# Optimization experiments

Measured on AMD Instinct MI355X. Metric: run time of the kernel, lower is better.

## Reference

```python
import jax, jax.numpy as jnp
import numpy as np

N = 100000      # nodes
K = 16          # sampled neighbors per node (aggregate_num)
D = 256         # features_dim
DO = 256        # out_feat_dim
ALPHA = 0.2     # LeakyReLU negative slope (args.alpha)
EPS = 1e-12     # F.normalize eps


def setup_inputs() -> dict:
    key = jax.random.key(0)
    k1, k2, k3 = jax.random.split(key, 3)
    h = jax.random.normal(k1, (N, D), dtype=jnp.float32)
    neighbors = jax.random.randint(k2, (N, K), 0, N, dtype=jnp.int64)
    # Xavier-uniform-ish init for W_gcn
    limit = float(np.sqrt(6.0 / (D + DO)))
    W_gcn = jax.random.uniform(k3, (D, DO), dtype=jnp.float32, minval=-limit, maxval=limit)
    return {"h": h, "neighbors": neighbors, "W_gcn": W_gcn}


def reference(h, neighbors, W_gcn):
    # GCN-style aggregate: mean of self feature and K sampled neighbor features.
    # (dropout on neighbor feats is identity in eval mode)
    neigh_sum = jnp.sum(h[neighbors], axis=1)          # [N, D] gather + reduce
    agg = (h + neigh_sum) / jnp.float32(K + 1)         # [N, D]
    z = agg @ W_gcn                                    # [N, DO]
    z = jnp.where(z >= 0, z, ALPHA * z)                # LeakyReLU
    norm = jnp.sqrt(jnp.sum(z * z, axis=1, keepdims=True))
    return z / jnp.maximum(norm, EPS)                  # L2 normalize per row
```

## Files before the change

kernel.cpp:

```cpp
#include <hip/hip_runtime.h>
#include <stdint.h>

#define N_NODES 100000
#define KNBR 16
#define ALPHA 0.2f

typedef __attribute__((ext_vector_type(8))) short bf16x8;
typedef __attribute__((ext_vector_type(4))) float f32x4;
typedef __attribute__((ext_vector_type(4))) unsigned int u32x4;
typedef unsigned short u16;
typedef unsigned int u32;
typedef unsigned char u8;

static __device__ __forceinline__ u16 f2bf(float f) {
  u32 u = __builtin_bit_cast(u32, f);
  u += 0x7fffu + ((u >> 16) & 1u);
  return (u16)(u >> 16);
}

__global__ __launch_bounds__(256) void prep_w_kernel(const float* __restrict__ W,
                                                     u16* __restrict__ Wb) {
  const int t = blockIdx.x * 256 + threadIdx.x;
  const int l = t & 63;
  const int ct = (t >> 6) & 15;
  const int ks = t >> 10;
  const int colbase = ct * 16 + (l & 15);
  const int k0 = ks * 32 + (l >> 4) * 8;
  u32 wq[4];
#pragma unroll
  for (int q = 0; q < 4; ++q) {
    const u16 b0 = f2bf(W[(k0 + 2 * q) * 256 + colbase]);
    const u16 b1 = f2bf(W[(k0 + 2 * q + 1) * 256 + colbase]);
    wq[q] = (u32)b0 | ((u32)b1 << 16);
  }
  u32x4 o = {wq[0], wq[1], wq[2], wq[3]};
  *(u32x4*)(Wb + (size_t)t * 8) = o;
}

__global__ __launch_bounds__(256, 4) void gemm_kernel(const float* __restrict__ h,
                                                      const u16* __restrict__ Wb,
                                                      u8* __restrict__ Yq,
                                                      float* __restrict__ scale) {
  __shared__ __align__(16) u16 aS[32 * 256];
  __shared__ float redS[4][32];
  __shared__ float invSS[32];
  const int tid = threadIdx.x;
  const int blk = blockIdx.x;
  const size_t base = (size_t)blk * (32 * 256);

#pragma unroll
  for (int i = 0; i < 8; ++i) {
    const int flat = i * 1024 + tid * 4;
    const int row = flat >> 8, d0 = flat & 255;
    const f32x4 v = __builtin_nontemporal_load((const f32x4*)(h + base + flat));
    uint2 o;
    asm("v_cvt_pk_bf16_f32 %0, %1, %2" : "=v"(o.x) : "v"(v[0]), "v"(v[1]));
    asm("v_cvt_pk_bf16_f32 %0, %1, %2" : "=v"(o.y) : "v"(v[2]), "v"(v[3]));
    *(uint2*)((char*)aS + row * 512 + ((d0 * 2) ^ ((row & 7) << 4))) = o;
  }
  __syncthreads();

  const int l = tid & 63, wv = tid >> 6;
  const int l15 = l & 15, lg = l >> 4;
  f32x4 acc[2][4] = {};
  const u32x4* wbL = ((const u32x4*)Wb) + (size_t)(wv * 4) * 64 + l;
  const char* aggB = (const char*)aS;
  const int rb0 = l15 * 512;
  const int xm = (l15 & 7) << 4;
#pragma unroll 2
  for (int ks = 0; ks < 8; ++ks) {
    const int offk = ((ks * 64) + lg * 16) ^ xm;
    const bf16x8 a0 = *(const bf16x8*)(aggB + rb0 + offk);
    const bf16x8 a1 = *(const bf16x8*)(aggB + rb0 + 8192 + offk);
#pragma unroll
    for (int c = 0; c < 4; ++c) {
      const u32x4 bw = wbL[ks * 1024 + c * 64];
      const bf16x8 b = __builtin_bit_cast(bf16x8, bw);
      acc[0][c] = __builtin_amdgcn_mfma_f32_16x16x32_bf16(a0, b, acc[0][c], 0, 0, 0);
      acc[1][c] = __builtin_amdgcn_mfma_f32_16x16x32_bf16(a1, b, acc[1][c], 0, 0, 0);
    }
  }

#pragma unroll
  for (int rt = 0; rt < 2; ++rt)
#pragma unroll
    for (int j = 0; j < 4; ++j) {
      float m = 0.f;
#pragma unroll
      for (int c = 0; c < 4; ++c) m = fmaxf(m, fabsf(acc[rt][c][j]));
      m = fmaxf(m, __shfl_xor(m, 1)); m = fmaxf(m, __shfl_xor(m, 2));
      m = fmaxf(m, __shfl_xor(m, 4)); m = fmaxf(m, __shfl_xor(m, 8));
      redS[wv][rt * 16 + lg * 4 + j] = m;
    }
  __syncthreads();
  if (tid < 32) {
    float m = fmaxf(fmaxf(redS[0][tid], redS[1][tid]),
                    fmaxf(redS[2][tid], redS[3][tid]));
    m = fmaxf(m, 1e-20f);
    scale[blk * 32 + tid] = m * (1.0f / 127.0f);
    invSS[tid] = 127.0f / m;
  }
  __syncthreads();

  u8* qS = (u8*)aS;
#pragma unroll
  for (int rt = 0; rt < 2; ++rt)
#pragma unroll
    for (int j = 0; j < 4; ++j) {
      const int r = rt * 16 + lg * 4 + j;
      const float inv = invSS[r];
      const int sw = ((r >> 2) & 7) << 5;
#pragma unroll
      for (int c = 0; c < 4; ++c) {
        float t = fmaf(acc[rt][c][j], inv, 128.5f);
        t = fminf(255.f, fmaxf(1.f, t));
        qS[r * 256 + ((wv * 64 + c * 16 + l15) ^ sw)] = (u8)(u32)t;
      }
    }
  __syncthreads();

  const u32x4* q4 = (const u32x4*)aS;
  u32x4* yg = (u32x4*)(Yq + (size_t)blk * 8192);
#pragma unroll
  for (int q = 0; q < 2; ++q) {
    const int f = q * 4096 + tid * 16;
    const int row = f >> 8, col = f & 255;
    const int colx = col ^ (((row >> 2) & 7) << 5);
    __builtin_nontemporal_store(q4[(row * 256 + colx) >> 4], (u32x4*)&yg[f >> 4]);
  }
}

__global__ __launch_bounds__(256) void gather_kernel(const u8* __restrict__ Yq,
                                                     const float* __restrict__ scale,
                                                     const int* __restrict__ nbr,
                                                     float* __restrict__ out) {
  const int tid = threadIdx.x;
  const int lane = tid & 63, wv = tid >> 6;
  const int node = __builtin_amdgcn_readfirstlane(blockIdx.x * 4 + wv);

  const int il = nbr[node * KNBR + (lane & 15)];
  const float vscale = scale[il];
  const float sself = scale[node];
  const u32* yb = (const u32*)Yq;

  u32 v[17];
  v[0] = yb[(size_t)node * 64 + lane];
#pragma unroll
  for (int j = 0; j < 16; ++j) {
    const int r = __builtin_amdgcn_readlane(il, j);
    v[j + 1] = yb[(size_t)r * 64 + lane];
  }

  float a0, a1, a2, a3, S = sself;
  {
    float f0, f1, f2, f3;
    asm("v_cvt_f32_ubyte0 %0, %1" : "=v"(f0) : "v"(v[0]));
    asm("v_cvt_f32_ubyte1 %0, %1" : "=v"(f1) : "v"(v[0]));
    asm("v_cvt_f32_ubyte2 %0, %1" : "=v"(f2) : "v"(v[0]));
    asm("v_cvt_f32_ubyte3 %0, %1" : "=v"(f3) : "v"(v[0]));
    a0 = sself * f0; a1 = sself * f1; a2 = sself * f2; a3 = sself * f3;
  }
#pragma unroll
  for (int j = 0; j < 16; ++j) {
    const float s = __builtin_bit_cast(
        float, __builtin_amdgcn_readlane(__builtin_bit_cast(int, vscale), j));
    float f0, f1, f2, f3;
    asm("v_cvt_f32_ubyte0 %0, %1" : "=v"(f0) : "v"(v[j + 1]));
    asm("v_cvt_f32_ubyte1 %0, %1" : "=v"(f1) : "v"(v[j + 1]));
    asm("v_cvt_f32_ubyte2 %0, %1" : "=v"(f2) : "v"(v[j + 1]));
    asm("v_cvt_f32_ubyte3 %0, %1" : "=v"(f3) : "v"(v[j + 1]));
    S += s;
    a0 = fmaf(s, f0, a0); a1 = fmaf(s, f1, a1);
    a2 = fmaf(s, f2, a2); a3 = fmaf(s, f3, a3);
  }
  const float sc = 1.0f / 17.0f, bias = 128.0f * S;
  a0 = (a0 - bias) * sc; a1 = (a1 - bias) * sc;
  a2 = (a2 - bias) * sc; a3 = (a3 - bias) * sc;
  a0 = (a0 >= 0.f) ? a0 : ALPHA * a0;
  a1 = (a1 >= 0.f) ? a1 : ALPHA * a1;
  a2 = (a2 >= 0.f) ? a2 : ALPHA * a2;
  a3 = (a3 >= 0.f) ? a3 : ALPHA * a3;

  float ss = a0 * a0 + a1 * a1 + a2 * a2 + a3 * a3;
  ss += __shfl_xor(ss, 1);  ss += __shfl_xor(ss, 2);
  ss += __shfl_xor(ss, 4);  ss += __shfl_xor(ss, 8);
  ss += __shfl_xor(ss, 16); ss += __shfl_xor(ss, 32);
  const float inv = 1.0f / fmaxf(sqrtf(ss), 1e-12f);

  f32x4 o = {a0 * inv, a1 * inv, a2 * inv, a3 * inv};
  __builtin_nontemporal_store(o, (f32x4*)(out + (size_t)node * 256 + lane * 4));
}

extern "C" void kernel_launch(void* const* d_in, const int* in_sizes, int n_in,
                              void* d_out, int out_size, void* d_ws, size_t ws_size,
                              hipStream_t stream) {
  const float* h = (const float*)d_in[0];
  const int* nbr = (const int*)d_in[1];
  const float* W = (const float*)d_in[2];
  float* out = (float*)d_out;

  char* ws = (char*)d_ws;
  u16* Wb = (u16*)ws;
  float* scale = (float*)(ws + (1 << 17));
  u8* Yq = (u8*)(ws + (1 << 20));

  prep_w_kernel<<<32, 256, 0, stream>>>(W, Wb);
  gemm_kernel<<<N_NODES / 32, 256, 0, stream>>>(h, Wb, Yq, scale);
  gather_kernel<<<N_NODES / 4, 256, 0, stream>>>(Yq, scale, nbr, out);
}
```

Measured before the change: 114.3 us.

## Load A fragments directly from global, compute full output rows per wave

The GEMM kernel drops the LDS staging of h and the cross-wave reductions. Each wave now owns 16 rows and all 256 output columns, loading fp32 A fragments straight from global and converting them to bf16 in registers. It quantizes rows with a per-wave max and writes Yq directly, with no __syncthreads. The Yq column layout changes (interleaved by groups of 16), and the gather kernel's output store is remapped to match using scalar stores. This trades LDS traffic and barriers for more accumulator registers (64 floats), lower occupancy, uncoalesced strided A loads, and scattered 4-byte stores.

```diff
diff --git a/kernel.cpp b/kernel.cpp
--- a/kernel.cpp
+++ b/kernel.cpp
@@ -37,96 +37,65 @@
   *(u32x4*)(Wb + (size_t)t * 8) = o;
 }
 
-__global__ __launch_bounds__(256, 4) void gemm_kernel(const float* __restrict__ h,
+__global__ __launch_bounds__(256, 3) void gemm_kernel(const float* __restrict__ h,
                                                       const u16* __restrict__ Wb,
                                                       u8* __restrict__ Yq,
                                                       float* __restrict__ scale) {
-  __shared__ __align__(16) u16 aS[32 * 256];
-  __shared__ float redS[4][32];
-  __shared__ float invSS[32];
   const int tid = threadIdx.x;
-  const int blk = blockIdx.x;
-  const size_t base = (size_t)blk * (32 * 256);
-
-#pragma unroll
-  for (int i = 0; i < 8; ++i) {
-    const int flat = i * 1024 + tid * 4;
-    const int row = flat >> 8, d0 = flat & 255;
-    const f32x4 v = __builtin_nontemporal_load((const f32x4*)(h + base + flat));
-    uint2 o;
-    asm("v_cvt_pk_bf16_f32 %0, %1, %2" : "=v"(o.x) : "v"(v[0]), "v"(v[1]));
-    asm("v_cvt_pk_bf16_f32 %0, %1, %2" : "=v"(o.y) : "v"(v[2]), "v"(v[3]));
-    *(uint2*)((char*)aS + row * 512 + ((d0 * 2) ^ ((row & 7) << 4))) = o;
-  }
-  __syncthreads();
-
   const int l = tid & 63, wv = tid >> 6;
   const int l15 = l & 15, lg = l >> 4;
-  f32x4 acc[2][4] = {};
-  const u32x4* wbL = ((const u32x4*)Wb) + (size_t)(wv * 4) * 64 + l;
-  const char* aggB = (const char*)aS;
-  const int rb0 = l15 * 512;
-  const int xm = (l15 & 7) << 4;
-#pragma unroll 2
+  const int rowb = blockIdx.x * 64 + wv * 16;
+  int arow = rowb + l15;
+  if (arow >= N_NODES) arow = N_NODES - 1;
+  const float* hrow = h + (size_t)arow * 256;
+  const u32x4* wb = (const u32x4*)Wb;
+
+  f32x4 acc[16] = {};
+#pragma unroll
   for (int ks = 0; ks < 8; ++ks) {
-    const int offk = ((ks * 64) + lg * 16) ^ xm;
-    const bf16x8 a0 = *(const bf16x8*)(aggB + rb0 + offk);
-    const bf16x8 a1 = *(const bf16x8*)(aggB + rb0 + 8192 + offk);
+    const f32x4 a0 = __builtin_nontemporal_load((const f32x4*)(hrow + ks * 32 + lg * 8));
+    const f32x4 a1 = __builtin_nontemporal_load((const f32x4*)(hrow + ks * 32 + lg * 8 + 4));
+    u32 p0, p1, p2, p3;
+    asm("v_cvt_pk_bf16_f32 %0, %1, %2" : "=v"(p0) : "v"(a0[0]), "v"(a0[1]));
+    asm("v_cvt_pk_bf16_f32 %0, %1, %2" : "=v"(p1) : "v"(a0[2]), "v"(a0[3]));
+    asm("v_cvt_pk_bf16_f32 %0, %1, %2" : "=v"(p2) : "v"(a1[0]), "v"(a1[1]));
+    asm("v_cvt_pk_bf16_f32 %0, %1, %2" : "=v"(p3) : "v"(a1[2]), "v"(a1[3]));
+    u32x4 au = {p0, p1, p2, p3};
+    const bf16x8 a = __builtin_bit_cast(bf16x8, au);
 #pragma unroll
-    for (int c = 0; c < 4; ++c) {
-      const u32x4 bw = wbL[ks * 1024 + c * 64];
+    for (int c = 0; c < 16; ++c) {
+      const u32x4 bw = wb[(size_t)(ks * 16 + c) * 64 + l];
       const bf16x8 b = __builtin_bit_cast(bf16x8, bw);
-      acc[0][c] = __builtin_amdgcn_mfma_f32_16x16x32_bf16(a0, b, acc[0][c], 0, 0, 0);
-      acc[1][c] = __builtin_amdgcn_mfma_f32_16x16x32_bf16(a1, b, acc[1][c], 0, 0, 0);
+      acc[c] = __builtin_amdgcn_mfma_f32_16x16x32_bf16(a, b, acc[c], 0, 0, 0);
     }
   }
 
 #pragma unroll
-  for (int rt = 0; rt < 2; ++rt)
+  for (int j = 0; j < 4; ++j) {
+    float m = 0.f;
 #pragma unroll
-    for (int j = 0; j < 4; ++j) {
-      float m = 0.f;
+    for (int c = 0; c < 16; ++c) m = fmaxf(m, fabsf(acc[c][j]));
+    m = fmaxf(m, __shfl_xor(m, 1)); m = fmaxf(m, __shfl_xor(m, 2));
+    m = fmaxf(m, __shfl_xor(m, 4)); m = fmaxf(m, __shfl_xor(m, 8));
+    m = fmaxf(m, 1e-20f);
+    const float invj = 127.0f / m;
+
+    const int r = rowb + lg * 4 + j;
+    if (r < N_NODES) {
+      if (l15 == 0) scale[r] = m * (1.0f / 127.0f);
+      u8* yr = Yq + (size_t)r * 256 + l15 * 4;
 #pragma unroll
-      for (int c = 0; c < 4; ++c) m = fmaxf(m, fabsf(acc[rt][c][j]));
-      m = fmaxf(m, __shfl_xor(m, 1)); m = fmaxf(m, __shfl_xor(m, 2));
-      m = fmaxf(m, __shfl_xor(m, 4)); m = fmaxf(m, __shfl_xor(m, 8));
-      redS[wv][rt * 16 + lg * 4 + j] = m;
-    }
-  __syncthreads();
-  if (tid < 32) {
-    float m = fmaxf(fmaxf(redS[0][tid], redS[1][tid]),
-                    fmaxf(redS[2][tid], redS[3][tid]));
-    m = fmaxf(m, 1e-20f);
-    scale[blk * 32 + tid] = m * (1.0f / 127.0f);
-    invSS[tid] = 127.0f / m;
-  }
-  __syncthreads();
-
-  u8* qS = (u8*)aS;
+      for (int g = 0; g < 4; ++g) {
+        u32 pk = 0;
 #pragma unroll
-  for (int rt = 0; rt < 2; ++rt)
-#pragma unroll
-    for (int j = 0; j < 4; ++j) {
-      const int r = rt * 16 + lg * 4 + j;
-      const float inv = invSS[r];
-      const int sw = ((r >> 2) & 7) << 5;
-#pragma unroll
-      for (int c = 0; c < 4; ++c) {
-        float t = fmaf(acc[rt][c][j], inv, 128.5f);
-        t = fminf(255.f, fmaxf(1.f, t));
-        qS[r * 256 + ((wv * 64 + c * 16 + l15) ^ sw)] = (u8)(u32)t;
+        for (int c4 = 0; c4 < 4; ++c4) {
+          float t = fmaf(acc[g * 4 + c4][j], invj, 128.5f);
+          t = fminf(255.f, fmaxf(1.f, t));
+          pk |= ((u32)(u8)(u32)t) << (8 * c4);
+        }
+        __builtin_nontemporal_store(pk, (u32*)(yr + g * 64));
       }
     }
-  __syncthreads();
-
-  const u32x4* q4 = (const u32x4*)aS;
-  u32x4* yg = (u32x4*)(Yq + (size_t)blk * 8192);
-#pragma unroll
-  for (int q = 0; q < 2; ++q) {
-    const int f = q * 4096 + tid * 16;
-    const int row = f >> 8, col = f & 255;
-    const int colx = col ^ (((row >> 2) & 7) << 5);
-    __builtin_nontemporal_store(q4[(row * 256 + colx) >> 4], (u32x4*)&yg[f >> 4]);
   }
 }
 
@@ -187,8 +156,12 @@
   ss += __shfl_xor(ss, 16); ss += __shfl_xor(ss, 32);
   const float inv = 1.0f / fmaxf(sqrtf(ss), 1e-12f);
 
-  f32x4 o = {a0 * inv, a1 * inv, a2 * inv, a3 * inv};
-  __builtin_nontemporal_store(o, (f32x4*)(out + (size_t)node * 256 + lane * 4));
+  const int g = lane >> 4, li = lane & 15;
+  float* op = out + (size_t)node * 256 + g * 64 + li;
+  __builtin_nontemporal_store(a0 * inv, op);
+  __builtin_nontemporal_store(a1 * inv, op + 16);
+  __builtin_nontemporal_store(a2 * inv, op + 32);
+  __builtin_nontemporal_store(a3 * inv, op + 48);
 }
 
 extern "C" void kernel_launch(void* const* d_in, const int* in_sizes, int n_in,
@@ -205,6 +178,6 @@
   u8* Yq = (u8*)(ws + (1 << 20));
 
   prep_w_kernel<<<32, 256, 0, stream>>>(W, Wb);
-  gemm_kernel<<<N_NODES / 32, 256, 0, stream>>>(h, Wb, Yq, scale);
+  gemm_kernel<<<(N_NODES + 63) / 64, 256, 0, stream>>>(h, Wb, Yq, scale);
   gather_kernel<<<N_NODES / 4, 256, 0, stream>>>(Yq, scale, nbr, out);
 }
```

Result: slower. 143.5 us (+25.6%).
